# Kernel optimization log

Measured on AMD Instinct MI355X. Metric: run time of the kernel, lower is better.

Reference implementation:

```python
import jax, jax.numpy as jnp
import numpy as np

KSIZE = 7       # patch size
STRIDE_Q = 4    # stride_1: query patch stride
STRIDE_KV = 1   # stride_2: key/value patch stride
SCALE = 10.0    # softmax_scale


def unfold(x, k, stride, pad):
    """torch.nn.Unfold equivalent. x:[B,C,H,W] -> [B, C*k*k, L] (c-major, then kh, kw)."""
    x = jnp.pad(x, ((0, 0), (0, 0), (pad, pad), (pad, pad)))
    B, C, Hp, Wp = x.shape
    nh = (Hp - k) // stride + 1
    nw = (Wp - k) // stride + 1
    sl = lambda i, n: slice(i, i + (n - 1) * stride + 1, stride)
    # [B, C, k*k, nh, nw]
    pat = jnp.stack([x[:, :, sl(i, nh), sl(j, nw)] for i in range(k) for j in range(k)], axis=2)
    return pat.reshape(B, C * k * k, nh * nw)


def fold(p, k, stride, pad, H, W):
    """torch.nn.functional.fold equivalent (overlap-add). p:[B, C*k*k, L] -> [B,C,H,W]."""
    B, D, L = p.shape
    C = D // (k * k)
    nh = (H + 2 * pad - k) // stride + 1
    nw = (W + 2 * pad - k) // stride + 1
    p = p.reshape(B, C, k, k, nh, nw)
    out = jnp.zeros((B, C, H + 2 * pad, W + 2 * pad), p.dtype)
    sl = lambda i, n: slice(i, i + (n - 1) * stride + 1, stride)
    for i in range(k):
        for j in range(k):
            out = out.at[:, :, sl(i, nh), sl(j, nw)].add(p[:, :, i, j])
    return out[:, :, pad:pad + H, pad:pad + W]


def conv1x1(x, w, bias):
    # w: [out, in]
    return jnp.einsum('bihw,oi->bohw', x, w) + bias[None, :, None, None]


def setup_inputs() -> dict:
    key = jax.random.key(0)
    ks = jax.random.split(key, 9)
    B, Cin, H, W = 4, 64, 128, 128
    Cit = 16
    s_in = 1.0 / np.sqrt(Cin)
    s_it = 1.0 / np.sqrt(Cit)
    return {
        'b': jax.random.normal(ks[0], (B, Cin, H, W), jnp.float32),
        'g_w': jax.random.normal(ks[1], (Cit, Cin), jnp.float32) * s_in,
        'g_b': jax.random.normal(ks[2], (Cit,), jnp.float32) * 0.01,
        'th_w': jax.random.normal(ks[3], (Cit, Cin), jnp.float32) * s_in,
        'th_b': jax.random.normal(ks[4], (Cit,), jnp.float32) * 0.01,
        'ph_w': jax.random.normal(ks[5], (Cit, Cin), jnp.float32) * s_in,
        'ph_b': jax.random.normal(ks[6], (Cit,), jnp.float32) * 0.01,
        'o_w': jax.random.normal(ks[7], (Cin, Cit), jnp.float32) * s_it,
        'o_b': jax.random.normal(ks[8], (Cin,), jnp.float32) * 0.01,
    }


def reference(b, g_w, g_b, th_w, th_b, ph_w, ph_b, o_w, o_b):
    B, Cin, H, W = b.shape
    pad = KSIZE // 2
    b1 = conv1x1(b, g_w, g_b)      # queries source  [B,16,H,W]
    b2 = conv1x1(b, th_w, th_b)    # values source
    b3 = conv1x1(b, ph_w, ph_b)    # keys source

    Q = unfold(b1, KSIZE, STRIDE_Q, pad).transpose(0, 2, 1)   # [B, L1, D]
    K = unfold(b3, KSIZE, STRIDE_KV, pad).transpose(0, 2, 1)  # [B, L2, D]
    V = unfold(b2, KSIZE, STRIDE_KV, pad).transpose(0, 2, 1)  # [B, L2, D]

    scores = jnp.einsum('bqd,bkd->bqk', Q, K)                 # [B, L1, L2]
    attn = jax.nn.softmax(scores * SCALE, axis=-1)
    Zp = jnp.einsum('bqk,bkd->bqd', attn, V).transpose(0, 2, 1)  # [B, D, L1]

    y = fold(Zp, KSIZE, STRIDE_Q, pad, H, W)                  # overlap-add
    Zc = fold(jnp.ones_like(Zp), KSIZE, STRIDE_Q, pad, H, W)  # overlap counts
    y = y / Zc
    y = conv1x1(y, o_w, o_b)
    return b + y
```

## Files before the change

### kernel.cpp

```cpp
#include <hip/hip_runtime.h>
#include <math.h>

#define NB 4
#define CIN 64
#define CIT 16
#define KS 7
#define PAD 3
#define HH 128
#define WW 128
#define HP 134
#define WPS 136
#define L1 1024
#define DD 784
#define SCALE_F 10.0f
#define WSCR 4.0f
#define TCAP 128

#define NPIX (HP * WPS)
#define NHWCF (NB * NPIX * CIT)

typedef __attribute__((ext_vector_type(4))) float f32x4;
typedef __attribute__((ext_vector_type(8))) short s16x8;
typedef __attribute__((ext_vector_type(4))) unsigned int u32x4;

__device__ __forceinline__ unsigned short f2bf(float f) {
    unsigned u = __float_as_uint(f);
    unsigned r = (u + 0x7FFFu + ((u >> 16) & 1u)) >> 16;
    return (unsigned short)r;
}

__global__ __launch_bounds__(256) void k_prep(
    const float* __restrict__ bin,
    const float* __restrict__ gw, const float* __restrict__ gb,
    const float* __restrict__ tw, const float* __restrict__ tb,
    const float* __restrict__ pw, const float* __restrict__ pb,
    float* __restrict__ b1f, float* __restrict__ b2f, float* __restrict__ b3f,
    unsigned short* __restrict__ b1n, unsigned short* __restrict__ b3n)
{
    int p = blockIdx.x * 256 + threadIdx.x;
    if (p >= NB * NPIX) return;
    int x = p % WPS; int r = p / WPS; int y = r % HP; int bb = r / HP;
    bool inter = (x >= PAD && x < PAD + WW && y >= PAD && y < PAD + HH);
    float v[CIN];
    if (inter) {
        int iy = y - PAD, ix = x - PAD;
        const float* src = bin + ((size_t)(bb * CIN) * HH + iy) * WW + ix;
        #pragma unroll
        for (int ci = 0; ci < CIN; ++ci) v[ci] = src[ci * HH * WW];
    }
    float a1v[CIT], a2v[CIT], a3v[CIT];
    unsigned short o1[CIT], o3[CIT];
    #pragma unroll
    for (int co = 0; co < CIT; ++co) {
        float a1 = 0.f, a2 = 0.f, a3 = 0.f;
        if (inter) {
            a1 = gb[co]; a2 = tb[co]; a3 = pb[co];
            #pragma unroll
            for (int ci = 0; ci < CIN; ++ci) {
                float vv = v[ci];
                a1 += gw[co * CIN + ci] * vv;
                a2 += tw[co * CIN + ci] * vv;
                a3 += pw[co * CIN + ci] * vv;
            }
        }
        a1v[co] = a1; a2v[co] = a2; a3v[co] = a3;
        o1[co] = f2bf(a1); o3[co] = f2bf(a3);
    }
    size_t pb16 = (size_t)p * CIT;
    #pragma unroll
    for (int g = 0; g < 4; ++g) {
        f32x4 w1 = {a1v[4*g], a1v[4*g+1], a1v[4*g+2], a1v[4*g+3]};
        f32x4 w2 = {a2v[4*g], a2v[4*g+1], a2v[4*g+2], a2v[4*g+3]};
        f32x4 w3 = {a3v[4*g], a3v[4*g+1], a3v[4*g+2], a3v[4*g+3]};
        *(f32x4*)(b1f + pb16 + 4*g) = w1;
        *(f32x4*)(b2f + pb16 + 4*g) = w2;
        *(f32x4*)(b3f + pb16 + 4*g) = w3;
    }
    unsigned pk1[8], pk3[8];
    #pragma unroll
    for (int kk = 0; kk < 8; ++kk) {
        pk1[kk] = (unsigned)o1[2 * kk] | ((unsigned)o1[2 * kk + 1] << 16);
        pk3[kk] = (unsigned)o3[2 * kk] | ((unsigned)o3[2 * kk + 1] << 16);
    }
    unsigned short* d1 = b1n + pb16;
    unsigned short* d3 = b3n + pb16;
    u32x4 w1a = {pk1[0], pk1[1], pk1[2], pk1[3]}, w1b = {pk1[4], pk1[5], pk1[6], pk1[7]};
    u32x4 w3a = {pk3[0], pk3[1], pk3[2], pk3[3]}, w3b = {pk3[4], pk3[5], pk3[6], pk3[7]};
    *(u32x4*)d1 = w1a; *(u32x4*)(d1 + 8) = w1b;
    *(u32x4*)d3 = w3a; *(u32x4*)(d3 + 8) = w3b;
}

__global__ __launch_bounds__(512, 2) void k_screen(
    const unsigned short* __restrict__ b1n, const unsigned short* __restrict__ b3n,
    _Float16* __restrict__ tmaxh)
{
    int blk = blockIdx.x;
    int qt = blk & 3;
    int qh = (blk >> 2) & 31;
    int bb = blk >> 7;
    int qstart_ky = qt * 32;
    int tid = threadIdx.x;
    int lane = tid & 63, w = tid >> 6;
    int lanelow = lane & 15;
    int h = (lane >> 5) & 1;
    int clo = (lane >> 4) & 1;

    __shared__ __align__(16) short smem[32 * 800];

    const unsigned short* b1nb = b1n + (size_t)bb * (NPIX * CIT);
    const unsigned short* b3nb = b3n + (size_t)bb * (NPIX * CIT);

    int qybase = 4 * qh;
    size_t tmbase0 = ((size_t)(bb * 64 + 2 * qh) * 4 + qt) * 4096;
    size_t tmbase1 = ((size_t)(bb * 64 + 2 * qh + 1) * 4 + qt) * 4096;

    for (int task = tid; task < 1600; task += 512) {
        int pp = task % 50, qq = task / 50;
        u32x4 lo = {0, 0, 0, 0}, hi = {0, 0, 0, 0};
        if (pp < 49) {
            int i = pp / 7, j = pp % 7;
            int qx = 4 * qq;
            const unsigned short* src = b1nb + ((size_t)(qybase + i) * WPS + qx + j) * CIT;
            lo = *(const u32x4*)src; hi = *(const u32x4*)(src + 8);
        }
        short* dst = smem + (qq * 50 + pp) * 16;
        *(u32x4*)dst = lo; *(u32x4*)(dst + 8) = hi;
    }
    __syncthreads();

    s16x8 B0[25], B1[25];
    #pragma unroll
    for (int s = 0; s < 25; ++s) {
        int ko = s * 32 + ((lane >> 4) & 3) * 8;
        B0[s] = *(const s16x8*)(smem + lanelow * 800 + ko);
        B1[s] = *(const s16x8*)(smem + (lanelow + 16) * 800 + ko);
    }
    __syncthreads();

    short* kring = smem;
    for (int task = tid; task < 8 * 268; task += 512) {
        int rr = task / 268, ch = task % 268;
        int row = qstart_ky + rr;
        *(u32x4*)(kring + rr * 2144 + ch * 8) =
            *(const u32x4*)(b3nb + (size_t)row * (WPS * CIT) + ch * 8);
    }
    __syncthreads();

    int abase = (w * 16 + lanelow) * 16 + clo * 8;

    for (int it = 0; it < 32; ++it) {
        int ky = qstart_ky + it;
        u32x4 pfA = {0, 0, 0, 0};
        bool hasPf = (it < 30) && (tid < 268);
        if (hasPf)
            pfA = *(const u32x4*)(b3nb + (size_t)(ky + 8) * (WPS * CIT) + tid * 8);

        f32x4 C0 = {0.f, 0.f, 0.f, 0.f}, C1 = {0.f, 0.f, 0.f, 0.f};
        #pragma unroll
        for (int s = 0; s < 25; ++s) {
            const int pe = 2 * s;
            const int po = (2 * s + 1 < 49) ? (2 * s + 1) : 0;
            const int ie = pe / 7, je = pe % 7;
            const int io = po / 7, jo = po % 7;
            int i_h = h ? io : ie;
            int j_h = h ? jo : je;
            int slot = (ky + i_h) & 7;
            const short* ap = kring + slot * 2144 + j_h * 16 + abase;
            s16x8 a0 = *(const s16x8*)ap;
            C0 = __builtin_amdgcn_mfma_f32_16x16x32_bf16(a0, B0[s], C0, 0, 0, 0);
            C1 = __builtin_amdgcn_mfma_f32_16x16x32_bf16(a0, B1[s], C1, 0, 0, 0);
        }
        float lm0 = fmaxf(fmaxf(C0[0], C0[1]), fmaxf(C0[2], C0[3]));
        lm0 = fmaxf(lm0, __shfl_xor(lm0, 16));
        lm0 = fmaxf(lm0, __shfl_xor(lm0, 32));
        float lm1 = fmaxf(fmaxf(C1[0], C1[1]), fmaxf(C1[2], C1[3]));
        lm1 = fmaxf(lm1, __shfl_xor(lm1, 16));
        lm1 = fmaxf(lm1, __shfl_xor(lm1, 32));
        if (lane < 16) {
            tmaxh[tmbase0 + (size_t)it * 128 + w * 16 + lane] = (_Float16)lm0;
            tmaxh[tmbase1 + (size_t)it * 128 + w * 16 + lane] = (_Float16)lm1;
        }
        __syncthreads();
        if (hasPf)
            *(u32x4*)(kring + ((ky + 8) & 7) * 2144 + tid * 8) = pfA;
        __syncthreads();
    }
}

__global__ __launch_bounds__(256) void k_finalize(
    const float* __restrict__ b1f, const float* __restrict__ b2f,
    const float* __restrict__ b3f, const _Float16* __restrict__ tmaxh,
    float* __restrict__ Zp)
{
    int wv = threadIdx.x >> 6;
    int lane = threadIdx.x & 63;
    int gq = blockIdx.x * 4 + wv;
    int bb = gq >> 10, q = gq & 1023;
    int qh = q >> 5, qw = q & 31;
    int qy = qh * 4, qx = qw * 4;
    int qidx = q & 15;
    int ch = lane & 15, pbase = lane >> 4;

    __shared__ int tq[4][TCAP];

    const float* b1b = b1f + (size_t)bb * (NPIX * CIT);
    const float* b2b = b2f + (size_t)bb * (NPIX * CIT);
    const float* b3b = b3f + (size_t)bb * (NPIX * CIT);

    const _Float16* tbq = tmaxh + (size_t)(bb * 64 + (q >> 4)) * 16384 + qidx;
    float tv[16]; float mg = -1e30f;
    #pragma unroll
    for (int k = 0; k < 16; ++k) {
        tv[k] = (float)tbq[16 * (lane + 64 * k)];
        mg = fmaxf(mg, tv[k]);
    }
    #pragma unroll
    for (int o = 32; o > 0; o >>= 1) mg = fmaxf(mg, __shfl_xor(mg, o));
    float thr = mg - WSCR;

    int cnt = 0;
    #pragma unroll
    for (int k = 0; k < 16; ++k) {
        bool p = (tv[k] >= thr);
        unsigned long long mk = __ballot(p);
        if (p) {
            int pos = cnt + (int)__popcll(mk & ((1ull << lane) - 1ull));
            if (pos < TCAP) tq[wv][pos] = lane + 64 * k;
        }
        cnt += (int)__popcll(mk);
    }
    int nt = min(cnt, TCAP);
    int n = nt * 16;
    __syncthreads();

    float qreg[13]; int offs[13];
    int qorg = (qy * WPS + qx) * CIT;
    #pragma unroll
    for (int k = 0; k < 13; ++k) {
        int p = pbase + 4 * k;
        if (p < 49) {
            int pi = p / 7, pj = p % 7;
            offs[k] = (pi * WPS + pj) * CIT + ch;
            qreg[k] = b1b[qorg + offs[k]];
        } else { offs[k] = 0; qreg[k] = 0.f; }
    }

    float m = -1e30f, l = 0.f, acc[13];
    #pragma unroll
    for (int k = 0; k < 13; ++k) acc[k] = 0.f;

    for (int ci0 = 0; ci0 < n; ci0 += 4) {
        int kb[4];
        #pragma unroll
        for (int u = 0; u < 4; ++u) {
            int ci = ci0 + u;
            int e = tq[wv][ci >> 4];
            int ky = (e >> 8) * 32 + ((e >> 3) & 31);
            int kx = (e & 7) * 16 + (ci & 15);
            kb[u] = (ky * WPS + kx) * CIT;
        }
        float kv[4][13], vv[4][13];
        #pragma unroll
        for (int u = 0; u < 4; ++u) {
            #pragma unroll
            for (int k = 0; k < 13; ++k) {
                kv[u][k] = b3b[kb[u] + offs[k]];
                vv[u][k] = b2b[kb[u] + offs[k]];
            }
        }
        float s[4];
        #pragma unroll
        for (int u = 0; u < 4; ++u) {
            float t = 0.f;
            #pragma unroll
            for (int k = 0; k < 13; ++k) t += qreg[k] * kv[u][k];
            #pragma unroll
            for (int o = 32; o > 0; o >>= 1) t += __shfl_xor(t, o);
            s[u] = t;
        }
        float mnew = fmaxf(m, fmaxf(fmaxf(s[0], s[1]), fmaxf(s[2], s[3])));
        float sc = __expf(SCALE_F * (m - mnew));
        float w0 = __expf(SCALE_F * (s[0] - mnew));
        float w1 = __expf(SCALE_F * (s[1] - mnew));
        float w2 = __expf(SCALE_F * (s[2] - mnew));
        float w3 = __expf(SCALE_F * (s[3] - mnew));
        l = l * sc + (w0 + w1 + w2 + w3);
        #pragma unroll
        for (int k = 0; k < 13; ++k)
            acc[k] = acc[k] * sc + w0 * vv[0][k] + w1 * vv[1][k]
                                 + w2 * vv[2][k] + w3 * vv[3][k];
        m = mnew;
    }

    float inv = (n > 0) ? (1.f / l) : 0.f;
    float* zq = Zp + (size_t)gq * DD;
    #pragma unroll
    for (int k = 0; k < 13; ++k) {
        int d = lane + 64 * k;
        if (d < DD) zq[d] = acc[k] * inv;
    }
}

__global__ __launch_bounds__(256) void k_fold(
    const float* __restrict__ bin, const float* __restrict__ ow,
    const float* __restrict__ ob, const float* __restrict__ Zp,
    float* __restrict__ outp)
{
    int p = blockIdx.x * 256 + threadIdx.x;
    if (p >= NB * HH * WW) return;
    int ox = p % WW; int r = p / WW; int oy = r % HH; int bb = r / HH;
    int yp = oy + PAD, xp = ox + PAD;
    int qh0 = (yp - 3) >> 2, qh1 = min(31, yp >> 2);
    int qw0 = (xp - 3) >> 2, qw1 = min(31, xp >> 2);
    float cnt = (float)((qh1 - qh0 + 1) * (qw1 - qw0 + 1));
    float y16[CIT];
    #pragma unroll
    for (int c = 0; c < CIT; ++c) y16[c] = 0.f;
    for (int qhh = qh0; qhh <= qh1; ++qhh) {
        int i = yp - 4 * qhh;
        for (int qww = qw0; qww <= qw1; ++qww) {
            int j = xp - 4 * qww;
            const float* zb = Zp + (size_t)((bb << 10) + qhh * 32 + qww) * DD + (i * 7 + j) * CIT;
            #pragma unroll
            for (int c = 0; c < CIT; ++c) y16[c] += zb[c];
        }
    }
    float icnt = 1.f / cnt;
    #pragma unroll
    for (int c = 0; c < CIT; ++c) y16[c] *= icnt;
    size_t oidx = ((size_t)(bb * CIN) * HH + oy) * WW + ox;
    for (int co = 0; co < CIN; ++co) {
        float a = ob[co];
        #pragma unroll
        for (int c = 0; c < CIT; ++c) a += ow[co * CIT + c] * y16[c];
        outp[oidx + (size_t)co * HH * WW] = bin[oidx + (size_t)co * HH * WW] + a;
    }
}

extern "C" void kernel_launch(void* const* d_in, const int* in_sizes, int n_in,
                              void* d_out, int out_size, void* d_ws, size_t ws_size,
                              hipStream_t stream) {
    (void)in_sizes; (void)n_in; (void)out_size; (void)ws_size;
    const float* bin = (const float*)d_in[0];
    const float* gw  = (const float*)d_in[1];
    const float* gb  = (const float*)d_in[2];
    const float* tw  = (const float*)d_in[3];
    const float* tb  = (const float*)d_in[4];
    const float* pw  = (const float*)d_in[5];
    const float* pb  = (const float*)d_in[6];
    const float* ow  = (const float*)d_in[7];
    const float* ob  = (const float*)d_in[8];

    float* outp = (float*)d_out;
    float* b3f = outp;
    float* b1f = outp + NHWCF;
    unsigned short* b3n = (unsigned short*)(outp + 2 * (size_t)NHWCF);
    unsigned short* b1n = b3n + NHWCF;

    float* ws = (float*)d_ws;
    float* b2f = ws;
    float* Zp  = ws + NHWCF;
    _Float16* tmaxh = (_Float16*)(ws + NHWCF + (size_t)NB * L1 * DD);

    hipLaunchKernelGGL(k_prep, dim3((NB * NPIX + 255) / 256), dim3(256), 0, stream,
                       bin, gw, gb, tw, tb, pw, pb, b1f, b2f, b3f, b1n, b3n);
    hipLaunchKernelGGL(k_screen, dim3(512), dim3(512), 0, stream,
                       b1n, b3n, tmaxh);
    hipLaunchKernelGGL(k_finalize, dim3(1024), dim3(256), 0, stream,
                       b1f, b2f, b3f, tmaxh, Zp);
    hipLaunchKernelGGL(k_fold, dim3((NB * HH * WW + 255) / 256), dim3(256), 0, stream,
                       bin, ow, ob, Zp, outp);
}
```

Baseline: 234.6 us.

## Batch K-row ring refills in screen kernel and transpose tile-max layout

The screen kernel's key-row ring grows from 8 to 16 rows with a padded row stride. Rows are now refilled eight at a time after each group of eight iterations, instead of one row per iteration with two barriers each, and MFMA phases run at raised wave priority. The tile-max output layout is transposed so each query's 1024 tile maxima are contiguous, letting the finalize kernel read them with two 16-byte vector loads instead of 16 strided scalar loads. The trade-off is more LDS per block, which may lower occupancy, and bulk refills that stall the waves rather than overlapping with compute.

```diff
diff --git a/kernel.cpp b/kernel.cpp
--- a/kernel.cpp
+++ b/kernel.cpp
@@ -18,6 +18,7 @@
 
 #define NPIX (HP * WPS)
 #define NHWCF (NB * NPIX * CIT)
+#define RSTR 2176
 
 typedef __attribute__((ext_vector_type(4))) float f32x4;
 typedef __attribute__((ext_vector_type(8))) short s16x8;
@@ -105,14 +106,14 @@
     int h = (lane >> 5) & 1;
     int clo = (lane >> 4) & 1;
 
-    __shared__ __align__(16) short smem[32 * 800];
+    __shared__ __align__(16) short smem[16 * RSTR];
 
     const unsigned short* b1nb = b1n + (size_t)bb * (NPIX * CIT);
     const unsigned short* b3nb = b3n + (size_t)bb * (NPIX * CIT);
 
     int qybase = 4 * qh;
-    size_t tmbase0 = ((size_t)(bb * 64 + 2 * qh) * 4 + qt) * 4096;
-    size_t tmbase1 = ((size_t)(bb * 64 + 2 * qh + 1) * 4 + qt) * 4096;
+    size_t qb0 = ((size_t)((bb * 64 + 2 * qh) * 16 + lanelow)) * 1024 + qt * 256 + w;
+    size_t qb1 = ((size_t)((bb * 64 + 2 * qh + 1) * 16 + lanelow)) * 1024 + qt * 256 + w;
 
     for (int task = tid; task < 1600; task += 512) {
         int pp = task % 50, qq = task / 50;
@@ -138,52 +139,59 @@
     __syncthreads();
 
     short* kring = smem;
-    for (int task = tid; task < 8 * 268; task += 512) {
-        int rr = task / 268, ch = task % 268;
-        int row = qstart_ky + rr;
-        *(u32x4*)(kring + rr * 2144 + ch * 8) =
-            *(const u32x4*)(b3nb + (size_t)row * (WPS * CIT) + ch * 8);
+    for (int task = tid; task < 16 * 272; task += 512) {
+        int rr = task / 272, ch = task % 272;
+        *(u32x4*)(kring + rr * RSTR + ch * 8) =
+            *(const u32x4*)(b3nb + (size_t)(qstart_ky + rr) * (WPS * CIT) + ch * 8);
     }
     __syncthreads();
 
     int abase = (w * 16 + lanelow) * 16 + clo * 8;
 
-    for (int it = 0; it < 32; ++it) {
-        int ky = qstart_ky + it;
-        u32x4 pfA = {0, 0, 0, 0};
-        bool hasPf = (it < 30) && (tid < 268);
-        if (hasPf)
-            pfA = *(const u32x4*)(b3nb + (size_t)(ky + 8) * (WPS * CIT) + tid * 8);
-
-        f32x4 C0 = {0.f, 0.f, 0.f, 0.f}, C1 = {0.f, 0.f, 0.f, 0.f};
-        #pragma unroll
-        for (int s = 0; s < 25; ++s) {
-            const int pe = 2 * s;
-            const int po = (2 * s + 1 < 49) ? (2 * s + 1) : 0;
-            const int ie = pe / 7, je = pe % 7;
-            const int io = po / 7, jo = po % 7;
-            int i_h = h ? io : ie;
-            int j_h = h ? jo : je;
-            int slot = (ky + i_h) & 7;
-            const short* ap = kring + slot * 2144 + j_h * 16 + abase;
-            s16x8 a0 = *(const s16x8*)ap;
-            C0 = __builtin_amdgcn_mfma_f32_16x16x32_bf16(a0, B0[s], C0, 0, 0, 0);
-            C1 = __builtin_amdgcn_mfma_f32_16x16x32_bf16(a0, B1[s], C1, 0, 0, 0);
-        }
-        float lm0 = fmaxf(fmaxf(C0[0], C0[1]), fmaxf(C0[2], C0[3]));
-        lm0 = fmaxf(lm0, __shfl_xor(lm0, 16));
-        lm0 = fmaxf(lm0, __shfl_xor(lm0, 32));
-        float lm1 = fmaxf(fmaxf(C1[0], C1[1]), fmaxf(C1[2], C1[3]));
-        lm1 = fmaxf(lm1, __shfl_xor(lm1, 16));
-        lm1 = fmaxf(lm1, __shfl_xor(lm1, 32));
-        if (lane < 16) {
-            tmaxh[tmbase0 + (size_t)it * 128 + w * 16 + lane] = (_Float16)lm0;
-            tmaxh[tmbase1 + (size_t)it * 128 + w * 16 + lane] = (_Float16)lm1;
-        }
+    for (int p = 0; p < 4; ++p) {
+        __builtin_amdgcn_s_setprio(1);
+        for (int it8 = 0; it8 < 8; ++it8) {
+            int it = 8 * p + it8;
+            int ky = qstart_ky + it;
+            f32x4 C0 = {0.f, 0.f, 0.f, 0.f}, C1 = {0.f, 0.f, 0.f, 0.f};
+            #pragma unroll
+            for (int s = 0; s < 25; ++s) {
+                const int pe = 2 * s;
+                const int po = (2 * s + 1 < 49) ? (2 * s + 1) : 0;
+                const int ie = pe / 7, je = pe % 7;
+                const int io = po / 7, jo = po % 7;
+                int i_h = h ? io : ie;
+                int j_h = h ? jo : je;
+                int slot = (ky + i_h) & 15;
+                const short* ap = kring + slot * RSTR + j_h * 16 + abase;
+                s16x8 a0 = *(const s16x8*)ap;
+                C0 = __builtin_amdgcn_mfma_f32_16x16x32_bf16(a0, B0[s], C0, 0, 0, 0);
+                C1 = __builtin_amdgcn_mfma_f32_16x16x32_bf16(a0, B1[s], C1, 0, 0, 0);
+            }
+            float lm0 = fmaxf(fmaxf(C0[0], C0[1]), fmaxf(C0[2], C0[3]));
+            lm0 = fmaxf(lm0, __shfl_xor(lm0, 16));
+            lm0 = fmaxf(lm0, __shfl_xor(lm0, 32));
+            float lm1 = fmaxf(fmaxf(C1[0], C1[1]), fmaxf(C1[2], C1[3]));
+            lm1 = fmaxf(lm1, __shfl_xor(lm1, 16));
+            lm1 = fmaxf(lm1, __shfl_xor(lm1, 32));
+            if (lane < 16) {
+                tmaxh[qb0 + it * 8] = (_Float16)lm0;
+                tmaxh[qb1 + it * 8] = (_Float16)lm1;
+            }
+        }
+        __builtin_amdgcn_s_setprio(0);
         __syncthreads();
-        if (hasPf)
-            *(u32x4*)(kring + ((ky + 8) & 7) * 2144 + tid * 8) = pfA;
-        __syncthreads();
+        if (p < 3) {
+            int rbase = qstart_ky + 8 * p + 16;
+            for (int task = tid; task < 8 * 272; task += 512) {
+                int rr = task / 272, ch = task % 272;
+                int row = rbase + rr;
+                int srow = (row < HP) ? row : (HP - 1);
+                *(u32x4*)(kring + (row & 15) * RSTR + ch * 8) =
+                    *(const u32x4*)(b3nb + (size_t)srow * (WPS * CIT) + ch * 8);
+            }
+            __syncthreads();
+        }
     }
 }
 
@@ -198,7 +206,6 @@
     int bb = gq >> 10, q = gq & 1023;
     int qh = q >> 5, qw = q & 31;
     int qy = qh * 4, qx = qw * 4;
-    int qidx = q & 15;
     int ch = lane & 15, pbase = lane >> 4;
 
     __shared__ int tq[4][TCAP];
@@ -207,11 +214,14 @@
     const float* b2b = b2f + (size_t)bb * (NPIX * CIT);
     const float* b3b = b3f + (size_t)bb * (NPIX * CIT);
 
-    const _Float16* tbq = tmaxh + (size_t)(bb * 64 + (q >> 4)) * 16384 + qidx;
+    const _Float16* qb = tmaxh + ((size_t)((bb * 64 + (q >> 4)) * 16 + (q & 15))) * 1024;
+    _Float16 tvh[16];
+    *(u32x4*)&tvh[0] = *(const u32x4*)(qb + (size_t)lane * 16);
+    *(u32x4*)&tvh[8] = *(const u32x4*)(qb + (size_t)lane * 16 + 8);
     float tv[16]; float mg = -1e30f;
     #pragma unroll
     for (int k = 0; k < 16; ++k) {
-        tv[k] = (float)tbq[16 * (lane + 64 * k)];
+        tv[k] = (float)tvh[k];
         mg = fmaxf(mg, tv[k]);
     }
     #pragma unroll
@@ -225,7 +235,7 @@
         unsigned long long mk = __ballot(p);
         if (p) {
             int pos = cnt + (int)__popcll(mk & ((1ull << lane) - 1ull));
-            if (pos < TCAP) tq[wv][pos] = lane + 64 * k;
+            if (pos < TCAP) tq[wv][pos] = lane * 16 + k;
         }
         cnt += (int)__popcll(mk);
     }
```

Result: no change. 230.8 us (-1.6%).
